# Kernel tuning notes

Hardware: AMD Instinct MI355X
Metric: run time of the kernel (lower is better)

The kernel has to match this reference:

```python
import jax, jax.numpy as jnp
import numpy as np

EPS = 1e-12  # torch F.normalize default eps

def l2norm(x, axis):
    n = jnp.sqrt(jnp.sum(x * x, axis=axis, keepdims=True))
    return x / jnp.maximum(n, EPS)

def conv2d(x, w, b, pad):
    y = jax.lax.conv_general_dilated(x, w, (1, 1), [(pad, pad), (pad, pad)],
                                     dimension_numbers=('NCHW', 'OIHW', 'NCHW'))
    return y + b[None, :, None, None]

def setup_inputs() -> dict:
    key = jax.random.key(0)
    ks = jax.random.split(key, 12)
    N, C, H, W, K = 16, 256, 64, 64, 32
    s = 0.05
    return {
        'feature':   jax.random.normal(ks[0], (N, C, H, W), jnp.float32),
        'conv_up_w': jax.random.normal(ks[1], (K, C, 3, 3), jnp.float32) * s,
        'conv_up_b': jax.random.normal(ks[2], (K,), jnp.float32) * s,
        'centroids': jax.random.uniform(ks[3], (K, C), jnp.float32),
        'upfc_w':    jax.random.normal(ks[4], (C, K * C), jnp.float32) * s,
        'upfc_b':    jax.random.normal(ks[5], (C,), jnp.float32) * s,
        't1_w':      jax.random.normal(ks[6], (C, 2 * C, 1, 1), jnp.float32) * s,
        't1_b':      jax.random.normal(ks[7], (C,), jnp.float32) * s,
        't2_w':      jax.random.normal(ks[8], (C, C, 1, 1), jnp.float32) * s,
        't2_b':      jax.random.normal(ks[9], (C,), jnp.float32) * s,
    }

def reference(feature, conv_up_w, conv_up_b, centroids, upfc_w, upfc_b, t1_w, t1_b, t2_w, t2_b):
    N, C, H, W = feature.shape
    K = centroids.shape[0]
    # --- UP branch ---
    xn = l2norm(feature, axis=1)                       # (N,C,H,W)
    sa = jax.nn.softmax(conv2d(xn, conv_up_w, conv_up_b, 1), axis=1)  # (N,K,H,W)
    sa_flat = sa.reshape(N, K, H * W)                  # (N,K,L)
    x_flat = xn.reshape(N, C, H * W)                   # (N,C,L)
    # sum_l sa[n,k,l] * (x[n,c,l] - centroid[k,c])  ==  two matmuls, no (N,K,C,L) tensor
    up = jnp.einsum('nkl,ncl->nkc', sa_flat, x_flat) \
         - jnp.sum(sa_flat, axis=-1)[:, :, None] * centroids[None]   # (N,K,C)
    up = l2norm(up, axis=2).reshape(N, K * C)
    up = l2norm(up, axis=1)
    up = up @ upfc_w.T + upfc_b                        # (N,C)
    up_map = jnp.broadcast_to(up[:, :, None, None], (N, C, H, W))
    # --- transform ---
    nf = jnp.concatenate([feature, up_map], axis=1)    # (N,2C,H,W)
    h = jax.nn.relu(conv2d(nf, t1_w, t1_b, 0))
    return jax.nn.relu(conv2d(h, t2_w, t2_b, 0))
```

## Files before the change

### kernel.cpp

```cpp
#include <hip/hip_runtime.h>
#include <cstdint>

#define N_ 16
#define C_ 256
#define H_ 64
#define W_ 64
#define L_ 4096
#define K_ 32
#define CL_ (C_*L_)
#define KL_ (K_*L_)
#define KC_ (K_*C_)

typedef __attribute__((ext_vector_type(8))) short short8;
typedef __attribute__((ext_vector_type(4))) float f32x4;

__device__ __forceinline__ unsigned short f2bf(float x) {
    unsigned int u = __float_as_uint(x);
    u += 0x7fffu + ((u >> 16) & 1u);
    return (unsigned short)(u >> 16);
}
__device__ __forceinline__ unsigned int pack2(float a, float b) {
    return (unsigned int)f2bf(a) | ((unsigned int)f2bf(b) << 16);
}

__device__ __forceinline__ void glds16(const void* g, void* l) {
    __builtin_amdgcn_global_load_lds(
        (const __attribute__((address_space(1))) unsigned int*)g,
        (__attribute__((address_space(3))) unsigned int*)l, 16, 0, 0);
}

__global__ __launch_bounds__(256) void k_prep(
    const float* __restrict__ f, float* __restrict__ rinv,
    float* __restrict__ snorm, unsigned short* __restrict__ xnb)
{
    __shared__ float tile[256 * 34];
    __shared__ float ssred[8 * 33];
    __shared__ float rbuf[32];
    int bid = blockIdx.x;
    int n = bid >> 7;
    int l0 = (bid & 127) << 5;
    int tid = threadIdx.x;
    int l = tid & 31, cb = tid >> 5;
    const float* fp = f + (size_t)n * CL_ + l0 + l;
    float ss = 0.f;
#pragma unroll
    for (int i = 0; i < 32; ++i) {
        int c = (cb << 5) + i;
        float v = fp[(size_t)c * L_];
        tile[c * 34 + l] = v;
        ss = fmaf(v, v, ss);
    }
    ssred[cb * 33 + l] = ss;
    __syncthreads();
    if (tid < 32) {
        float s = 0.f;
#pragma unroll
        for (int j = 0; j < 8; ++j) s += ssred[j * 33 + tid];
        float sq = fmaxf(sqrtf(s), 1e-12f);
        float ri = 1.0f / sq;
        rinv[n * L_ + l0 + tid] = ri;
        snorm[n * L_ + l0 + tid] = sq;
        rbuf[tid] = ri;
    }
    __syncthreads();
    float ri = rbuf[l];
    unsigned short* op = xnb + ((size_t)n * L_ + l0 + l) * C_ + (cb << 5);
#pragma unroll
    for (int g = 0; g < 4; ++g) {
        unsigned int pk[4];
#pragma unroll
        for (int d = 0; d < 4; ++d) {
            int c = (cb << 5) + (g << 3) + (d << 1);
            pk[d] = pack2(tile[c * 34 + l] * ri, tile[(c + 1) * 34 + l] * ri);
        }
        *(uint4*)(op + (g << 3)) = make_uint4(pk[0], pk[1], pk[2], pk[3]);
    }
}

__global__ __launch_bounds__(256) void k_wpack(const float* __restrict__ w, unsigned short* __restrict__ wb) {
    int i = blockIdx.x * 256 + threadIdx.x;
    int j = i & 7;
    int k = (i >> 3) & 31;
    int q = (i >> 8) & 3;
    int ch = (i >> 10) & 7;
    int t = i >> 13;
    int c = (ch << 5) + (q << 3) + j;
    wb[i] = f2bf(w[k * 2304 + c * 9 + t]);
}

__global__ __launch_bounds__(256) void k_wpackp(const float* __restrict__ w, int stride,
                                                unsigned short* __restrict__ wb2) {
    int i = blockIdx.x * 256 + threadIdx.x;
    int j = i & 7, co = (i >> 3) & 255, q = (i >> 11) & 3, ch = i >> 13;
    int ci = (ch << 5) + (q << 3) + j;
    wb2[i] = f2bf(w[(size_t)co * stride + ci]);
}

__global__ __launch_bounds__(128, 2) void k_conv(
    const unsigned short* __restrict__ xnb, const unsigned short* __restrict__ wb,
    const float* __restrict__ bias, const float* __restrict__ zpad,
    float* __restrict__ sa, float* __restrict__ ssum)
{
    __shared__ __align__(16) unsigned short lsB[2][408 * 8];
    __shared__ __align__(16) unsigned short lsW[2][1152 * 8];
    __shared__ float sred[2][32];
    int bid = blockIdx.x;
    int n = bid & 15, y = (bid >> 4) & 63, px_b = bid >> 10;
    int tid = threadIdx.x;
    int wv = tid >> 6, lane = tid & 63;
    int r = lane & 15, quad = lane >> 4;
    int pxw = (wv << 4) + r;
    int xbase = (px_b << 5) - 1;
    const unsigned short* xb = xnb + (size_t)n * CL_;
    const unsigned short* zp = (const unsigned short*)zpad;

    const unsigned short* bsrc[4];
    bool bact[4];
#pragma unroll
    for (int k = 0; k < 4; ++k) {
        int c = (wv << 6) + (k << 7) + lane;
        bool act = c < 408;
        int cc = act ? c : 0;
        int row = cc / 136;
        int rem = cc - row * 136;
        int q = rem / 34;
        int px = rem - q * 34;
        int yy = y + row - 1, xx = xbase + px;
        bool ok = act && ((unsigned)yy < 64u) && ((unsigned)xx < 64u);
        bsrc[k] = ok ? (xb + (((size_t)(yy << 6) + xx) << 8) + (q << 3)) : zp;
        bact[k] = act;
    }

    f32x4 acc0 = (f32x4){0.f, 0.f, 0.f, 0.f};
    f32x4 acc1 = (f32x4){0.f, 0.f, 0.f, 0.f};

    {
#pragma unroll
        for (int k = 0; k < 4; ++k)
            if (bact[k]) glds16(bsrc[k], lsB[0] + (((wv << 6) + (k << 7)) << 3));
#pragma unroll
        for (int k = 0; k < 9; ++k) {
            int idx = wv * 9 + k;
            int t = idx >> 1, h = idx & 1;
            glds16(wb + (t << 13) + (h << 9) + (lane << 3), lsW[0] + (idx << 9));
        }
    }

    for (int i = 0; i < 8; ++i) {
        asm volatile("s_waitcnt vmcnt(0)" ::: "memory");
        __syncthreads();
        if (i < 7) {
            int c1 = (i + 1) << 5;
            unsigned short* dB = lsB[(i + 1) & 1];
            unsigned short* dW = lsW[(i + 1) & 1];
#pragma unroll
            for (int k = 0; k < 4; ++k)
                if (bact[k]) glds16(bsrc[k] + c1, dB + (((wv << 6) + (k << 7)) << 3));
#pragma unroll
            for (int k = 0; k < 9; ++k) {
                int idx = wv * 9 + k;
                int t = idx >> 1, h = idx & 1;
                glds16(wb + (t << 13) + (h << 9) + ((i + 1) << 10) + (lane << 3),
                       dW + (idx << 9));
            }
        }
        const unsigned short* bufB = lsB[i & 1];
        const unsigned short* bufW = lsW[i & 1];
#pragma unroll
        for (int dy = 0; dy < 3; ++dy) {
#pragma unroll
            for (int dx = 0; dx < 3; ++dx) {
                int t = dy * 3 + dx;
                short8 B  = *(const short8*)(bufB + ((((dy << 2) + quad) * 34 + (pxw + dx)) << 3));
                short8 A0 = *(const short8*)(bufW + (((t << 7) + (quad << 5) + r) << 3));
                short8 A1 = *(const short8*)(bufW + (((t << 7) + (quad << 5) + 16 + r) << 3));
                acc0 = __builtin_amdgcn_mfma_f32_16x16x32_bf16(A0, B, acc0, 0, 0, 0);
                acc1 = __builtin_amdgcn_mfma_f32_16x16x32_bf16(A1, B, acc1, 0, 0, 0);
            }
        }
    }
    float4 b0 = *(const float4*)(bias + (quad << 2));
    float4 b1 = *(const float4*)(bias + 16 + (quad << 2));
    float v[8];
    v[0] = acc0[0] + b0.x; v[1] = acc0[1] + b0.y; v[2] = acc0[2] + b0.z; v[3] = acc0[3] + b0.w;
    v[4] = acc1[0] + b1.x; v[5] = acc1[1] + b1.y; v[6] = acc1[2] + b1.z; v[7] = acc1[3] + b1.w;
    float mx = v[0];
#pragma unroll
    for (int j = 1; j < 8; ++j) mx = fmaxf(mx, v[j]);
    mx = fmaxf(mx, __shfl_xor(mx, 16));
    mx = fmaxf(mx, __shfl_xor(mx, 32));
    float s = 0.f;
#pragma unroll
    for (int j = 0; j < 8; ++j) { v[j] = __expf(v[j] - mx); s += v[j]; }
    s += __shfl_xor(s, 16);
    s += __shfl_xor(s, 32);
    float rs = 1.0f / s;
    float sv8[8];
#pragma unroll
    for (int j = 0; j < 8; ++j) sv8[j] = v[j] * rs;
    int l = (y << 6) + (px_b << 5) + pxw;
    float* sp = sa + (size_t)n * KL_ + l;
#pragma unroll
    for (int j = 0; j < 4; ++j) {
        sp[(size_t)((quad << 2) + j) * L_] = sv8[j];
        sp[(size_t)(16 + (quad << 2) + j) * L_] = sv8[4 + j];
    }
#pragma unroll
    for (int j = 0; j < 8; ++j) {
        float a = sv8[j];
        a += __shfl_xor(a, 1); a += __shfl_xor(a, 2);
        a += __shfl_xor(a, 4); a += __shfl_xor(a, 8);
        sv8[j] = a;
    }
    if (r == 0) {
#pragma unroll
        for (int j = 0; j < 4; ++j) {
            sred[wv][(quad << 2) + j] = sv8[j];
            sred[wv][16 + (quad << 2) + j] = sv8[4 + j];
        }
    }
    __syncthreads();
    if (tid < 32) {
        float t = sred[0][tid] + sred[1][tid];
        atomicAdd(ssum + n * K_ + tid, t);
    }
}

__global__ __launch_bounds__(256) void k_einsum(
    const float* __restrict__ f, const float* __restrict__ rinv,
    const float* __restrict__ sa, float* __restrict__ up)
{
    __shared__ float xn_s[C_ * 33];
    __shared__ float sa_s[K_ * 32];
    int bid = blockIdx.x;
    int n = bid >> 5;
    int l0 = (bid & 31) << 7;
    int tid = threadIdx.x;
    int kq = tid >> 5, cq = tid & 31;
    float acc[4][8];
#pragma unroll
    for (int i = 0; i < 4; ++i)
#pragma unroll
        for (int j = 0; j < 8; ++j) acc[i][j] = 0.f;

    for (int ch = 0; ch < 4; ++ch) {
        int lc = l0 + (ch << 5);
        __syncthreads();
        {
            int crow = tid >> 3, lq = (tid & 7) << 2;
#pragma unroll
            for (int p = 0; p < 8; ++p) {
                int c = (p << 5) + crow;
                float4 f4 = *(const float4*)(f + (size_t)n * CL_ + (size_t)c * L_ + lc + lq);
                float4 r4 = *(const float4*)(rinv + n * L_ + lc + lq);
                float* d = xn_s + c * 33 + lq;
                d[0] = f4.x * r4.x; d[1] = f4.y * r4.y; d[2] = f4.z * r4.z; d[3] = f4.w * r4.w;
            }
        }
        {
            int k = tid >> 3, lq = (tid & 7) << 2;
            float4 a4 = *(const float4*)(sa + (size_t)n * KL_ + (size_t)k * L_ + lc + lq);
            *(float4*)(sa_s + (k << 5) + lq) = a4;
        }
        __syncthreads();
#pragma unroll 4
        for (int l = 0; l < 32; ++l) {
            float sv[4], xv[8];
#pragma unroll
            for (int i = 0; i < 4; ++i) sv[i] = sa_s[((kq << 2) + i) * 32 + l];
#pragma unroll
            for (int j = 0; j < 8; ++j) xv[j] = xn_s[(cq + (j << 5)) * 33 + l];
#pragma unroll
            for (int i = 0; i < 4; ++i)
#pragma unroll
                for (int j = 0; j < 8; ++j) acc[i][j] = fmaf(sv[i], xv[j], acc[i][j]);
        }
    }
    float* upp = up + (size_t)n * KC_;
#pragma unroll
    for (int i = 0; i < 4; ++i)
#pragma unroll
        for (int j = 0; j < 8; ++j)
            atomicAdd(upp + ((kq << 2) + i) * C_ + cq + (j << 5), acc[i][j]);
}

__global__ __launch_bounds__(256) void k_rowfix(
    const float* __restrict__ up, const float* __restrict__ ssum,
    const float* __restrict__ cent, float* __restrict__ upn, float* __restrict__ rowss)
{
    __shared__ float red[256];
    int bid = blockIdx.x;
    int k = bid & 31;
    float sv = ssum[bid];
    float v = up[(size_t)bid * C_ + threadIdx.x] - sv * cent[k * C_ + threadIdx.x];
    red[threadIdx.x] = v * v; __syncthreads();
    for (int st = 128; st > 0; st >>= 1) {
        if (threadIdx.x < st) red[threadIdx.x] += red[threadIdx.x + st];
        __syncthreads();
    }
    float ss = red[0];
    float ri = 1.0f / fmaxf(sqrtf(ss), 1e-12f);
    upn[(size_t)bid * C_ + threadIdx.x] = v * ri;
    if (threadIdx.x == 0) rowss[bid] = ss * ri * ri;
}

__global__ __launch_bounds__(256) void k_fc(
    const float* __restrict__ upn, const float* __restrict__ rowss,
    const float* __restrict__ w, const float* __restrict__ b,
    float* __restrict__ upvec)
{
    __shared__ float rnb[16];
    __shared__ float red[16][5];
    int c = blockIdx.x;
    int tid = threadIdx.x;
    int wv = tid >> 6, lane = tid & 63;
    if (tid < 16) {
        float ts = 0.f;
#pragma unroll
        for (int k = 0; k < K_; ++k) ts += rowss[(tid << 5) + k];
        rnb[tid] = 1.0f / fmaxf(sqrtf(ts), 1e-12f);
    }
    float acc[16];
#pragma unroll
    for (int n = 0; n < 16; ++n) acc[n] = 0.f;
    const float* wr = w + (size_t)c * KC_;
#pragma unroll
    for (int g = 0; g < 8; ++g) {
        int kc = (g << 10) + (tid << 2);
        float4 w4 = *(const float4*)(wr + kc);
#pragma unroll
        for (int n = 0; n < 16; ++n) {
            float4 u4 = *(const float4*)(upn + n * KC_ + kc);
            acc[n] += w4.x * u4.x + w4.y * u4.y + w4.z * u4.z + w4.w * u4.w;
        }
    }
#pragma unroll
    for (int n = 0; n < 16; ++n) {
        float a = acc[n];
#pragma unroll
        for (int s = 1; s < 64; s <<= 1) a += __shfl_xor(a, s);
        if (lane == 0) red[n][wv] = a;
    }
    __syncthreads();
    if (tid < 16) {
        float v = red[tid][0] + red[tid][1] + red[tid][2] + red[tid][3];
        upvec[tid * C_ + c] = v * rnb[tid] + b[c];
    }
}

__global__ __launch_bounds__(256) void k_t1up(
    const float* __restrict__ upvec, const float* __restrict__ t1w,
    const float* __restrict__ t1b, float* __restrict__ t1up)
{
    __shared__ float wld[256];
    int co = blockIdx.x;
    int tid = threadIdx.x;
    wld[tid] = t1w[(size_t)co * 512 + 256 + tid];
    __syncthreads();
    int n = tid >> 4, s = tid & 15;
    float a = 0.f;
#pragma unroll
    for (int i = 0; i < 16; ++i)
        a += wld[s + (i << 4)] * upvec[n * C_ + s + (i << 4)];
#pragma unroll
    for (int st = 1; st < 16; st <<= 1) a += __shfl_xor(a, st);
    if (s == 0) t1up[n * C_ + co] = a + t1b[co];
}

__global__ __launch_bounds__(512, 2) void k_gemm1(
    const unsigned short* __restrict__ xnb, const unsigned short* __restrict__ wb2,
    const float* __restrict__ t1up, const float* __restrict__ snorm,
    unsigned short* __restrict__ hb)
{
    __shared__ __align__(16) unsigned short lsB[2][512 * 8];
    __shared__ __align__(16) unsigned short lsW[2][1024 * 8];
    int bid = blockIdx.x;
    int n = bid & 15, px_b = bid >> 4;
    int l0 = px_b << 7;
    int tid = threadIdx.x;
    int wv = tid >> 6, lane = tid & 63;
    int r = lane & 15, quad = lane >> 4;
    int pxl = (wv >> 2) << 6;
    int co0 = (wv & 3) << 6;
    const unsigned short* xrow = xnb + ((size_t)n * L_ + l0) * C_;

    int cbi = (wv << 6) + lane;
    int bq = cbi >> 7, bpx = cbi & 127;
    const unsigned short* bsrc = xrow + (size_t)bpx * C_ + (bq << 3);

    glds16(bsrc, lsB[0] + (cbi << 3));
#pragma unroll
    for (int k = 0; k < 2; ++k) {
        int cw = (wv << 7) + (k << 6) + lane;
        glds16(wb2 + ((size_t)cw << 3), lsW[0] + (cw << 3));
    }

    f32x4 acc[4][4];
#pragma unroll
    for (int i = 0; i < 4; ++i)
#pragma unroll
        for (int j = 0; j < 4; ++j) acc[i][j] = (f32x4){0.f, 0.f, 0.f, 0.f};

    for (int i = 0; i < 8; ++i) {
        asm volatile("s_waitcnt vmcnt(0)" ::: "memory");
        __syncthreads();
        if (i < 7) {
            glds16(bsrc + ((i + 1) << 5), lsB[(i + 1) & 1] + (cbi << 3));
#pragma unroll
            for (int k = 0; k < 2; ++k) {
                int cw = (wv << 7) + (k << 6) + lane;
                glds16(wb2 + ((size_t)(((i + 1) << 10) + cw) << 3),
                       lsW[(i + 1) & 1] + (cw << 3));
            }
        }
        const unsigned short* bufB = lsB[i & 1];
        const unsigned short* bufW = lsW[i & 1];
        short8 A[4], B[4];
#pragma unroll
        for (int t = 0; t < 4; ++t)
            A[t] = *(const short8*)(bufW + (((quad << 8) + co0 + (t << 4) + r) << 3));
#pragma unroll
        for (int t = 0; t < 4; ++t)
            B[t] = *(const short8*)(bufB + (((quad << 7) + pxl + (t << 4) + r) << 3));
#pragma unroll
        for (int pxt = 0; pxt < 4; ++pxt)
#pragma unroll
            for (int cot = 0; cot < 4; ++cot)
                acc[pxt][cot] = __builtin_amdgcn_mfma_f32_16x16x32_bf16(A[cot], B[pxt], acc[pxt][cot], 0, 0, 0);
    }
#pragma unroll
    for (int pxt = 0; pxt < 4; ++pxt) {
        int px = l0 + pxl + (pxt << 4) + r;
        float sc = snorm[n * L_ + px];
        unsigned short* orow = hb + ((size_t)n * L_ + px) * C_;
#pragma unroll
        for (int cot = 0; cot < 4; ++cot) {
            int cb = co0 + (cot << 4) + (quad << 2);
            float4 bb = *(const float4*)(t1up + n * C_ + cb);
            unsigned int p0 = pack2(fmaxf(fmaf(acc[pxt][cot][0], sc, bb.x), 0.f),
                                    fmaxf(fmaf(acc[pxt][cot][1], sc, bb.y), 0.f));
            unsigned int p1 = pack2(fmaxf(fmaf(acc[pxt][cot][2], sc, bb.z), 0.f),
                                    fmaxf(fmaf(acc[pxt][cot][3], sc, bb.w), 0.f));
            *(uint2*)(orow + cb) = make_uint2(p0, p1);
        }
    }
}

__global__ __launch_bounds__(256) void k_gemm2(
    const unsigned short* __restrict__ hb, const unsigned short* __restrict__ wb2,
    const float* __restrict__ t2b, float* __restrict__ out)
{
    __shared__ __align__(16) unsigned short lsB[2][512 * 8];
    __shared__ __align__(16) unsigned short lsW[2][512 * 8];
    int bid = blockIdx.x;
    int co_b = bid & 1, px_b = (bid >> 1) & 31, n = bid >> 6;
    int l0 = px_b << 7;
    int tid = threadIdx.x;
    int wv = tid >> 6, lane = tid & 63;
    int r = lane & 15, quad = lane >> 4;
    int pxl = (wv >> 1) << 6;
    int co0l = (wv & 1) << 6;
    int co0 = (co_b << 7) + co0l;
    const unsigned short* hrow = hb + ((size_t)n * L_ + l0) * C_;

#pragma unroll
    for (int k = 0; k < 2; ++k) {
        glds16(hrow + (size_t)((k << 6) + lane) * C_ + (wv << 3),
               lsB[0] + (((wv << 7) + (k << 6)) << 3));
        glds16(wb2 + (((wv << 8) + (co_b << 7) + (k << 6) + lane) << 3),
               lsW[0] + (((wv << 7) + (k << 6)) << 3));
    }

    f32x4 acc[4][4];
#pragma unroll
    for (int i = 0; i < 4; ++i)
#pragma unroll
        for (int j = 0; j < 4; ++j) acc[i][j] = (f32x4){0.f, 0.f, 0.f, 0.f};

    for (int i = 0; i < 8; ++i) {
        asm volatile("s_waitcnt vmcnt(0)" ::: "memory");
        __syncthreads();
        if (i < 7) {
#pragma unroll
            for (int k = 0; k < 2; ++k) {
                glds16(hrow + (size_t)((k << 6) + lane) * C_ + ((i + 1) << 5) + (wv << 3),
                       lsB[(i + 1) & 1] + (((wv << 7) + (k << 6)) << 3));
                glds16(wb2 + ((((((i + 1) << 2) + wv) << 8) + (co_b << 7) + (k << 6) + lane) << 3),
                       lsW[(i + 1) & 1] + (((wv << 7) + (k << 6)) << 3));
            }
        }
        const unsigned short* bufB = lsB[i & 1];
        const unsigned short* bufW = lsW[i & 1];
        short8 A[4], B[4];
#pragma unroll
        for (int t = 0; t < 4; ++t)
            A[t] = *(const short8*)(bufW + (((quad << 7) + co0l + (t << 4) + r) << 3));
#pragma unroll
        for (int t = 0; t < 4; ++t)
            B[t] = *(const short8*)(bufB + (((quad << 7) + pxl + (t << 4) + r) << 3));
#pragma unroll
        for (int pxt = 0; pxt < 4; ++pxt)
#pragma unroll
            for (int cot = 0; cot < 4; ++cot)
                acc[pxt][cot] = __builtin_amdgcn_mfma_f32_16x16x32_bf16(A[cot], B[pxt], acc[pxt][cot], 0, 0, 0);
    }
#pragma unroll
    for (int pxt = 0; pxt < 4; ++pxt) {
        int px = l0 + pxl + (pxt << 4) + r;
#pragma unroll
        for (int cot = 0; cot < 4; ++cot) {
            int cb = co0 + (cot << 4) + (quad << 2);
            float4 bb = *(const float4*)(t2b + cb);
            out[((size_t)n * C_ + cb + 0) * L_ + px] = fmaxf(acc[pxt][cot][0] + bb.x, 0.f);
            out[((size_t)n * C_ + cb + 1) * L_ + px] = fmaxf(acc[pxt][cot][1] + bb.y, 0.f);
            out[((size_t)n * C_ + cb + 2) * L_ + px] = fmaxf(acc[pxt][cot][2] + bb.z, 0.f);
            out[((size_t)n * C_ + cb + 3) * L_ + px] = fmaxf(acc[pxt][cot][3] + bb.w, 0.f);
        }
    }
}

extern "C" void kernel_launch(void* const* d_in, const int* in_sizes, int n_in,
                              void* d_out, int out_size, void* d_ws, size_t ws_size,
                              hipStream_t stream)
{
    const float* feature = (const float*)d_in[0];
    const float* conv_w  = (const float*)d_in[1];
    const float* conv_b  = (const float*)d_in[2];
    const float* cent    = (const float*)d_in[3];
    const float* upfc_w  = (const float*)d_in[4];
    const float* upfc_b  = (const float*)d_in[5];
    const float* t1w     = (const float*)d_in[6];
    const float* t1b     = (const float*)d_in[7];
    const float* t2w     = (const float*)d_in[8];
    const float* t2b     = (const float*)d_in[9];

    float* ws = (float*)d_ws;
    unsigned short* xnb = (unsigned short*)ws;
    unsigned short* hb  = xnb;
    float* rest  = ws + 8388608;
    float* rinv  = rest;
    float* sa    = rinv + 65536;
    float* up    = sa + 2097152;
    float* ssum  = up + 131072;
    float* zpad  = ssum + 512;
    float* snorm = zpad + 512;
    float* upn   = snorm + 65536;
    float* rowss = upn + 131072;
    float* upvec = rowss + 512;
    float* t1up  = upvec + 4096;
    unsigned short* wbconv = (unsigned short*)upn;
    unsigned short* t1wb = (unsigned short*)sa;
    unsigned short* t2wb = t1wb + 65536;
    float* out = (float*)d_out;

    hipMemsetAsync(up, 0, (131072 + 512 + 512) * sizeof(float), stream);
    k_prep     <<<2048, 256, 0, stream>>>(feature, rinv, snorm, xnb);
    k_wpack    <<<288,  256, 0, stream>>>(conv_w, wbconv);
    k_conv     <<<2048, 128, 0, stream>>>(xnb, wbconv, conv_b, zpad, sa, ssum);
    k_einsum   <<<512,  256, 0, stream>>>(feature, rinv, sa, up);
    k_rowfix   <<<512,  256, 0, stream>>>(up, ssum, cent, upn, rowss);
    k_wpackp   <<<256,  256, 0, stream>>>(t1w, 512, t1wb);
    k_wpackp   <<<256,  256, 0, stream>>>(t2w, 256, t2wb);
    k_fc       <<<256,  256, 0, stream>>>(upn, rowss, upfc_w, upfc_b, upvec);
    k_t1up     <<<256,  256, 0, stream>>>(upvec, t1w, t1b, t1up);
    k_gemm1    <<<512,  512, 0, stream>>>(xnb, t1wb, t1up, snorm, hb);
    k_gemm2    <<<1024, 256, 0, stream>>>(hb, t2wb, t2b, out);
}
```

Baseline: 285.8 us.

## Feed einsum from bf16 normalized features and coalesce prep stores via LDS

```diff
diff --git a/kernel.cpp b/kernel.cpp
--- a/kernel.cpp
+++ b/kernel.cpp
@@ -30,8 +30,8 @@
 }
 
 __global__ __launch_bounds__(256) void k_prep(
-    const float* __restrict__ f, float* __restrict__ rinv,
-    float* __restrict__ snorm, unsigned short* __restrict__ xnb)
+    const float* __restrict__ f, float* __restrict__ snorm,
+    unsigned short* __restrict__ xnb)
 {
     __shared__ float tile[256 * 34];
     __shared__ float ssred[8 * 33];
@@ -57,14 +57,12 @@
 #pragma unroll
         for (int j = 0; j < 8; ++j) s += ssred[j * 33 + tid];
         float sq = fmaxf(sqrtf(s), 1e-12f);
-        float ri = 1.0f / sq;
-        rinv[n * L_ + l0 + tid] = ri;
         snorm[n * L_ + l0 + tid] = sq;
-        rbuf[tid] = ri;
+        rbuf[tid] = 1.0f / sq;
     }
     __syncthreads();
     float ri = rbuf[l];
-    unsigned short* op = xnb + ((size_t)n * L_ + l0 + l) * C_ + (cb << 5);
+    uint4 pk4[4];
 #pragma unroll
     for (int g = 0; g < 4; ++g) {
         unsigned int pk[4];
@@ -73,7 +71,20 @@
             int c = (cb << 5) + (g << 3) + (d << 1);
             pk[d] = pack2(tile[c * 34 + l] * ri, tile[(c + 1) * 34 + l] * ri);
         }
-        *(uint4*)(op + (g << 3)) = make_uint4(pk[0], pk[1], pk[2], pk[3]);
+        pk4[g] = make_uint4(pk[0], pk[1], pk[2], pk[3]);
+    }
+    __syncthreads();
+    unsigned int* rpk = (unsigned int*)tile;
+#pragma unroll
+    for (int g = 0; g < 4; ++g)
+        *(uint4*)(rpk + l * 132 + (cb << 4) + (g << 2)) = pk4[g];
+    __syncthreads();
+    int col16 = tid & 31, rw = tid >> 5;
+#pragma unroll
+    for (int m2 = 0; m2 < 4; ++m2) {
+        int row = (m2 << 3) + rw;
+        uint4 v = *(const uint4*)(rpk + row * 132 + (col16 << 2));
+        *(uint4*)(xnb + ((size_t)n * L_ + l0 + row) * C_ + (col16 << 3)) = v;
     }
 }
 
@@ -227,16 +238,17 @@
 }
 
 __global__ __launch_bounds__(256) void k_einsum(
-    const float* __restrict__ f, const float* __restrict__ rinv,
-    const float* __restrict__ sa, float* __restrict__ up)
-{
-    __shared__ float xn_s[C_ * 33];
+    const unsigned short* __restrict__ xnb, const float* __restrict__ sa,
+    float* __restrict__ up)
+{
+    __shared__ float xn_s[32 * 257];
     __shared__ float sa_s[K_ * 32];
     int bid = blockIdx.x;
     int n = bid >> 5;
     int l0 = (bid & 31) << 7;
     int tid = threadIdx.x;
     int kq = tid >> 5, cq = tid & 31;
+    int rw = tid >> 5, col16 = tid & 31;
     float acc[4][8];
 #pragma unroll
     for (int i = 0; i < 4; ++i)
@@ -246,16 +258,15 @@
     for (int ch = 0; ch < 4; ++ch) {
         int lc = l0 + (ch << 5);
         __syncthreads();
-        {
-            int crow = tid >> 3, lq = (tid & 7) << 2;
-#pragma unroll
-            for (int p = 0; p < 8; ++p) {
-                int c = (p << 5) + crow;
-                float4 f4 = *(const float4*)(f + (size_t)n * CL_ + (size_t)c * L_ + lc + lq);
-                float4 r4 = *(const float4*)(rinv + n * L_ + lc + lq);
-                float* d = xn_s + c * 33 + lq;
-                d[0] = f4.x * r4.x; d[1] = f4.y * r4.y; d[2] = f4.z * r4.z; d[3] = f4.w * r4.w;
-            }
+#pragma unroll
+        for (int m = 0; m < 4; ++m) {
+            int row = (m << 3) + rw;
+            uint4 v = *(const uint4*)(xnb + ((size_t)n * L_ + lc + row) * C_ + (col16 << 3));
+            float* d = xn_s + row * 257 + (col16 << 3);
+            d[0] = __uint_as_float(v.x << 16); d[1] = __uint_as_float(v.x & 0xffff0000u);
+            d[2] = __uint_as_float(v.y << 16); d[3] = __uint_as_float(v.y & 0xffff0000u);
+            d[4] = __uint_as_float(v.z << 16); d[5] = __uint_as_float(v.z & 0xffff0000u);
+            d[6] = __uint_as_float(v.w << 16); d[7] = __uint_as_float(v.w & 0xffff0000u);
         }
         {
             int k = tid >> 3, lq = (tid & 7) << 2;
@@ -269,7 +280,7 @@
 #pragma unroll
             for (int i = 0; i < 4; ++i) sv[i] = sa_s[((kq << 2) + i) * 32 + l];
 #pragma unroll
-            for (int j = 0; j < 8; ++j) xv[j] = xn_s[(cq + (j << 5)) * 33 + l];
+            for (int j = 0; j < 8; ++j) xv[j] = xn_s[l * 257 + cq + (j << 5)];
 #pragma unroll
             for (int i = 0; i < 4; ++i)
 #pragma unroll
@@ -554,10 +565,10 @@
     float* out = (float*)d_out;
 
     hipMemsetAsync(up, 0, (131072 + 512 + 512) * sizeof(float), stream);
-    k_prep     <<<2048, 256, 0, stream>>>(feature, rinv, snorm, xnb);
+    k_prep     <<<2048, 256, 0, stream>>>(feature, snorm, xnb);
     k_wpack    <<<288,  256, 0, stream>>>(conv_w, wbconv);
     k_conv     <<<2048, 128, 0, stream>>>(xnb, wbconv, conv_b, zpad, sa, ssum);
-    k_einsum   <<<512,  256, 0, stream>>>(feature, rinv, sa, up);
+    k_einsum   <<<512,  256, 0, stream>>>(xnb, sa, up);
     k_rowfix   <<<512,  256, 0, stream>>>(up, ssum, cent, upn, rowss);
     k_wpackp   <<<256,  256, 0, stream>>>(t1w, 512, t1wb);
     k_wpackp   <<<256,  256, 0, stream>>>(t2w, 256, t2wb);
```

Result: no change. 285.1 us (-0.3%).
